# Performance work log

Measured on AMD Instinct MI355X. Metric: run time of the kernel, lower is better.

## Reference

```python
import jax, jax.numpy as jnp
import numpy as np

B, S, T = 256, 120, 24   # batch, src frames, predicted frames
D, H = 216, 1024          # input_dim (24 joints x 3x3 rotmat), hidden_dim


def setup_inputs() -> dict:
    key = jax.random.key(0)
    ks = jax.random.split(key, 8)
    s = 0.05  # ~ init_weights uniform(-0.08, 0.08) scale
    return {
        "src": jax.random.normal(ks[0], (B, S, D), jnp.float32),
        "tgt": jax.random.normal(ks[1], (B, T, D), jnp.float32),
        "W_ih": jax.random.normal(ks[2], (4 * H, D), jnp.float32) * s,
        "W_hh": jax.random.normal(ks[3], (4 * H, H), jnp.float32) * s,
        "b_ih": jnp.zeros((4 * H,), jnp.float32),
        "b_hh": jnp.zeros((4 * H,), jnp.float32),
        "W_out": jax.random.normal(ks[4], (D, H), jnp.float32) * s,
        "b_out": jnp.zeros((D,), jnp.float32),
        "max_len": T,
    }


def reference(src, tgt, W_ih, W_hh, b_ih, b_hh, W_out, b_out, max_len):
    # Eval-mode forward: dropout = identity.
    # Encoder: teacher-forced (teacher_forcing_ratio=1.0 -> always feed src[t]).
    def cell(x, h, c):
        # PyTorch LSTM gate order: i, f, g, o
        gates = x @ W_ih.T + b_ih + h @ W_hh.T + b_hh  # [B, 4H]
        i, f, g, o = jnp.split(gates, 4, axis=-1)
        c = jax.nn.sigmoid(f) * c + jax.nn.sigmoid(i) * jnp.tanh(g)
        h = jax.nn.sigmoid(o) * jnp.tanh(c)
        return h, c

    b = src.shape[0]
    h0 = jnp.zeros((b, H), src.dtype)
    c0 = jnp.zeros((b, H), src.dtype)

    # Encoder over src, time-major [S, B, D]
    def enc_step(carry, x):
        h, c = carry
        h, c = cell(x, h, c)
        return (h, c), None

    (h, c), _ = jax.lax.scan(enc_step, (h0, c0), jnp.swapaxes(src, 0, 1))

    # Decoder: first input is last src frame, then feed back projected output
    def dec_step(carry, _):
        h, c, x = carry
        h, c = cell(x, h, c)
        out = h @ W_out.T + b_out  # [B, D]
        return (h, c, out), out

    _, outs = jax.lax.scan(dec_step, (h, c, src[:, -1, :]), None, length=max_len)
    return jnp.swapaxes(outs, 0, 1)  # [B, max_len, D]
```

## Files before the change

kernel.cpp:

```cpp
#include <hip/hip_runtime.h>
#include <hip/hip_bf16.h>

typedef unsigned short u16;
typedef unsigned int   u32;
typedef unsigned long long u64;
typedef __attribute__((ext_vector_type(4)))  float  f32x4;
typedef __attribute__((ext_vector_type(8)))  short  short8;
typedef __attribute__((ext_vector_type(16))) float  f32x16;

#define MB     256
#define SRCT   120
#define DECT   24
#define NSTEP  144
#define DIN    216
#define HDIM   1024
#define KXP    224
#define KA     1248
#define NGATE  4096
#define OUTD   216
#define NWG    256

#define OFF_SRCBF 0u
#define OFF_H     13762560u
#define OFF_XDEC  14811136u
#define OFF_WCAT  14925824u
#define OFF_WO    25149440u
#define OFF_BAR   25591808u

__device__ __forceinline__ u16 f2bf(float f) {
    union { float f; unsigned v; } c; c.f = f;
    return (u16)((c.v + 0x7FFFu + ((c.v >> 16) & 1u)) >> 16);
}
__device__ __forceinline__ float sigm(float x)  { return 1.0f / (1.0f + __expf(-x)); }
__device__ __forceinline__ float tanh_(float x) { return 1.0f - 2.0f / (1.0f + __expf(2.0f * x)); }

__device__ __forceinline__ void astore(u64* p, u64 v) {
    __hip_atomic_store(p, v, __ATOMIC_RELAXED, __HIP_MEMORY_SCOPE_AGENT);
}

__device__ __forceinline__ short8 ld_sc(const u16* p) {
    short8 r;
    asm volatile("global_load_dwordx4 %0, %1, off sc0 sc1" : "=v"(r) : "v"(p));
    return r;
}
template <int N>
__device__ __forceinline__ void vwait() {
    asm volatile("s_waitcnt vmcnt(%0)" :: "n"(N));
    __builtin_amdgcn_sched_barrier(0);
}

__device__ __forceinline__ void g_arrive(u32* slots, int k) {
    __syncthreads();
    if (threadIdx.x == 0)
        __hip_atomic_fetch_add(slots + (k & 63), 1u, __ATOMIC_RELAXED, __HIP_MEMORY_SCOPE_AGENT);
}
__device__ __forceinline__ void g_wait(u32* slots, int k) {
    if (threadIdx.x == 0) {
        const u32 tgt = 32u * (u32)((k >> 6) + 1);
        while (__hip_atomic_load(slots + (k & 63), __ATOMIC_RELAXED, __HIP_MEMORY_SCOPE_AGENT) < tgt)
            __builtin_amdgcn_s_sleep(1);
    }
    __syncthreads();
}

__global__ void prep_kernel(const float* __restrict__ src,
                            const float* __restrict__ W_ih,
                            const float* __restrict__ W_hh,
                            const float* __restrict__ W_out,
                            u16* __restrict__ srcbf, u16* __restrict__ H,
                            u16* __restrict__ Xd,    u16* __restrict__ Wcat,
                            u16* __restrict__ Wo,    u32* __restrict__ bar) {
    const int nS  = SRCT * 8 * 28 * 256;
    const int nW  = NGATE * KA;
    const int nWo = OUTD * HDIM;
    const int nH  = MB * HDIM;
    const int nXd = 8 * 28 * 256;
    const int nB  = 8 * 64;
    const int total = nS + nW + nWo + nH + nXd + nB;
    for (int i = blockIdx.x * blockDim.x + threadIdx.x; i < total; i += gridDim.x * blockDim.x) {
        if (i < nS) {
            int r = i & 255, i2 = i >> 8;
            int m = r >> 3, e = r & 7;
            int oct = i2 % 28, q = i2 / 28;
            int gi = q & 7, t = q >> 3;
            int col = oct * 8 + e, b = gi * 32 + m;
            srcbf[i] = (col < DIN) ? f2bf(src[((size_t)b * SRCT + t) * DIN + col]) : (u16)0;
        } else if (i < nS + nW) {
            int j = i - nS;
            int r = j / KA, col = j % KA;
            u16 v = 0;
            if (col < DIN)       v = f2bf(W_ih[(size_t)r * DIN + col]);
            else if (col >= KXP) v = f2bf(W_hh[(size_t)r * HDIM + (col - KXP)]);
            Wcat[j] = v;
        } else if (i < nS + nW + nWo) {
            int j = i - nS - nW;
            Wo[j] = f2bf(W_out[j]);
        } else if (i < nS + nW + nWo + nH) {
            H[i - nS - nW - nWo] = 0;
        } else if (i < nS + nW + nWo + nH + nXd) {
            Xd[i - nS - nW - nWo - nH] = 0;
        } else {
            bar[i - nS - nW - nWo - nH - nXd] = 0;
        }
    }
}

template <int J>
__device__ __forceinline__ void gate_issue(short8 (&av)[20], const u16* xb, const u16* hb,
                                           int ktb, int lo) {
    int kt = ktb + J;
    if (kt > 77) kt = 77;
    const int o2 = 2 * kt;
    const u16* base = (o2 < 28) ? (xb + o2 * 256) : (hb + (o2 - 28) * 256);
    av[J] = ld_sc(base + lo);
}
template <int J>
__device__ __forceinline__ void gate_pro(short8 (&av)[20], const u16* xb, const u16* hb,
                                         int ktb, int lo) {
    gate_issue<J>(av, xb, hb, ktb, lo);
    if constexpr (J + 1 < 8) gate_pro<J + 1>(av, xb, hb, ktb, lo);
}
template <int J>
__device__ __forceinline__ void gate_body(short8 (&av)[20], short8 (&Bf)[4][20], f32x16 (&acc)[4],
                                          const u16* xb, const u16* hb, int ktb, int lo) {
    if constexpr (J + 8 < 20) gate_issue<J + 8>(av, xb, hb, ktb, lo);
    vwait<(J + 8 < 20) ? 8 : (19 - J)>();
    acc[0] = __builtin_amdgcn_mfma_f32_32x32x16_bf16(av[J], Bf[0][J], acc[0], 0, 0, 0);
    acc[1] = __builtin_amdgcn_mfma_f32_32x32x16_bf16(av[J], Bf[1][J], acc[1], 0, 0, 0);
    acc[2] = __builtin_amdgcn_mfma_f32_32x32x16_bf16(av[J], Bf[2][J], acc[2], 0, 0, 0);
    acc[3] = __builtin_amdgcn_mfma_f32_32x32x16_bf16(av[J], Bf[3][J], acc[3], 0, 0, 0);
    if constexpr (J + 1 < 20) gate_body<J + 1>(av, Bf, acc, xb, hb, ktb, lo);
}

template <int J>
__device__ __forceinline__ void out_issue(short8 (&av)[16], const u16* hb, int kt0, int lo) {
    const int o2 = 2 * (kt0 + J);
    av[J] = ld_sc(hb + o2 * 256 + lo);
}
template <int J>
__device__ __forceinline__ void out_pro(short8 (&av)[16], const u16* hb, int kt0, int lo) {
    out_issue<J>(av, hb, kt0, lo);
    if constexpr (J + 1 < 8) out_pro<J + 1>(av, hb, kt0, lo);
}
template <int J>
__device__ __forceinline__ void out_body(short8 (&av)[16], f32x16& oacc, const u16* hb,
                                         const u16* wob, int kt0, int lo) {
    if constexpr (J + 8 < 16) out_issue<J + 8>(av, hb, kt0, lo);
    vwait<(J + 8 < 16) ? 8 : (15 - J)>();
    short8 bf = *(const short8*)(wob + (size_t)(kt0 + J) * 16);
    oacc = __builtin_amdgcn_mfma_f32_32x32x16_bf16(av[J], bf, oacc, 0, 0, 0);
    if constexpr (J + 1 < 16) out_body<J + 1>(av, oacc, hb, wob, kt0, lo);
}

__global__ void __launch_bounds__(256, 1)
lstm_persist(const u16* __restrict__ srcbf, u16* __restrict__ H,
             u16* __restrict__ Xd, const u16* __restrict__ Wcat,
             const u16* __restrict__ Wo,
             const float* __restrict__ b_ih, const float* __restrict__ b_hh,
             const float* __restrict__ b_out,
             float* __restrict__ dout, u32* __restrict__ bar)
{
    __shared__ __align__(16) float G2[16 * 32 * 36];
    __shared__ __align__(16) u16  Hx[4 * 32 * 8];
    __shared__ __align__(16) char lds_pad[8192];

    const int bid  = blockIdx.x;
    const int g    = bid & 7;
    const int s    = bid >> 3;
    const int b0   = g * 32;
    const int tid  = threadIdx.x;
    const int p    = tid >> 6;
    const int lane = tid & 63;
    const int l31  = lane & 31;
    const int kg   = lane >> 5;
    const int lo   = kg * 256 + l31 * 8;

    if (tid == 255) *(volatile char*)lds_pad = 0;

    u32* gslots = bar + g * 64;
    u16* Xdg = Xd + (size_t)g * 7168;

    const int ktb = p * 20 - (p == 3 ? 1 : 0);
    const int ktc = (p < 2) ? 20 : 19;

    short8 Bfrag[4][20];
#pragma unroll
    for (int gg = 0; gg < 4; ++gg) {
        const u16* pw = Wcat + (size_t)(gg * 1024 + s * 32 + l31) * KA + kg * 8;
#pragma unroll
        for (int j = 0; j < 20; ++j) {
            if (j < ktc) {
                int kt = ktb + j;
                Bfrag[gg][j] = *(const short8*)(pw + (size_t)kt * 16);
            } else {
                Bfrag[gg][j] = short8{};
            }
        }
    }

    const int cs = tid & 31;
    const int bq = tid >> 5;
    float creg[4] = {0.f, 0.f, 0.f, 0.f};
    const int hcg = s * 32 + cs;
    const float bI  = b_ih[hcg]        + b_hh[hcg];
    const float bF  = b_ih[1024 + hcg] + b_hh[1024 + hcg];
    const float bG_ = b_ih[2048 + hcg] + b_hh[2048 + hcg];
    const float bO  = b_ih[3072 + hcg] + b_hh[3072 + hcg];
    const float bOutv = (s < 7 && hcg < OUTD) ? b_out[hcg] : 0.f;

    for (int t = 0; t < NSTEP; ++t) {
        const u16* hb    = H + (size_t)(t & 1) * (MB * HDIM) + (size_t)g * 32768;
        u16*       HTn   = H + (size_t)((t + 1) & 1) * (MB * HDIM);
        const u16* hnext = HTn + (size_t)g * 32768;
        const u16* xb;
        if (t < SRCT)       xb = srcbf + (size_t)(t * 8 + g) * 7168;
        else if (t == SRCT) xb = srcbf + (size_t)((SRCT - 1) * 8 + g) * 7168;
        else                xb = Xdg;

        f32x16 acc[4] = {f32x16{}, f32x16{}, f32x16{}, f32x16{}};
        {
            short8 av[20];
            gate_pro<0>(av, xb, hb, ktb, lo);
            gate_body<0>(av, Bfrag, acc, xb, hb, ktb, lo);
        }
#pragma unroll
        for (int gg = 0; gg < 4; ++gg) {
#pragma unroll
            for (int rq = 0; rq < 4; ++rq) {
                f32x4 v;
                v[0] = acc[gg][rq * 4 + 0]; v[1] = acc[gg][rq * 4 + 1];
                v[2] = acc[gg][rq * 4 + 2]; v[3] = acc[gg][rq * 4 + 3];
                *(f32x4*)&G2[(size_t)((gg * 4 + p) * 32 + l31) * 36 + rq * 8 + kg * 4] = v;
            }
        }
        __syncthreads();

        {
            f32x4 sg[4];
#pragma unroll
            for (int gg = 0; gg < 4; ++gg) {
                f32x4 a = *(const f32x4*)&G2[(size_t)((gg * 4 + 0) * 32 + cs) * 36 + bq * 4];
#pragma unroll
                for (int pp = 1; pp < 4; ++pp)
                    a += *(const f32x4*)&G2[(size_t)((gg * 4 + pp) * 32 + cs) * 36 + bq * 4];
                sg[gg] = a;
            }
#pragma unroll
            for (int i = 0; i < 4; ++i) {
                float gi = sg[0][i] + bI, gf = sg[1][i] + bF;
                float gG = sg[2][i] + bG_, go = sg[3][i] + bO;
                float c = sigm(gf) * creg[i] + sigm(gi) * tanh_(gG);
                creg[i] = c;
                Hx[(cs >> 3) * 256 + (bq * 4 + i) * 8 + (cs & 7)] = f2bf(sigm(go) * tanh_(c));
            }
        }
        __syncthreads();
        astore((u64*)HTn + (size_t)g * 8192 + s * 256 + tid, ((const u64*)Hx)[tid]);

        if (t < SRCT) {
            g_arrive(gslots, t);
            g_wait(gslots, t);
        } else {
            const int d  = t - SRCT;
            const int k1 = SRCT + 2 * d;
            g_arrive(gslots, k1);
            g_wait(gslots, k1);
            if (s < 7) {
                f32x16 oacc = {};
                const int orow = (s * 32 + l31 < OUTD) ? (s * 32 + l31) : (OUTD - 1);
                const u16* wob = Wo + (size_t)orow * HDIM + kg * 8;
                short8 av2[16];
                out_pro<0>(av2, hnext, p * 16, lo);
                out_body<0>(av2, oacc, hnext, wob, p * 16, lo);
#pragma unroll
                for (int rq = 0; rq < 4; ++rq) {
                    f32x4 v;
                    v[0] = oacc[rq * 4 + 0]; v[1] = oacc[rq * 4 + 1];
                    v[2] = oacc[rq * 4 + 2]; v[3] = oacc[rq * 4 + 3];
                    *(f32x4*)&G2[(size_t)(p * 32 + l31) * 36 + rq * 8 + kg * 4] = v;
                }
            }
            __syncthreads();
            if (s < 7) {
                const int  ocol = s * 32 + cs;
                const bool real = ocol < OUTD;
                f32x4 S = *(const f32x4*)&G2[(size_t)(0 * 32 + cs) * 36 + bq * 4];
#pragma unroll
                for (int pp = 1; pp < 4; ++pp)
                    S += *(const f32x4*)&G2[(size_t)(pp * 32 + cs) * 36 + bq * 4];
#pragma unroll
                for (int i = 0; i < 4; ++i) {
                    float v = real ? (S[i] + bOutv) : 0.f;
                    Hx[(cs >> 3) * 256 + (bq * 4 + i) * 8 + (cs & 7)] = real ? f2bf(v) : (u16)0;
                    if (real)
                        dout[(size_t)(b0 + bq * 4 + i) * (DECT * OUTD) + (size_t)d * OUTD + ocol] = v;
                }
            }
            __syncthreads();
            if (s < 7)
                astore((u64*)Xdg + s * 256 + tid, ((const u64*)Hx)[tid]);
            if (t < NSTEP - 1) {
                g_arrive(gslots, k1 + 1);
                g_wait(gslots, k1 + 1);
            }
        }
    }
}

extern "C" void kernel_launch(void* const* d_in, const int* in_sizes, int n_in,
                              void* d_out, int out_size, void* d_ws, size_t ws_size,
                              hipStream_t stream) {
    const float* src   = (const float*)d_in[0];
    const float* W_ih  = (const float*)d_in[2];
    const float* W_hh  = (const float*)d_in[3];
    const float* b_ih  = (const float*)d_in[4];
    const float* b_hh  = (const float*)d_in[5];
    const float* W_out = (const float*)d_in[6];
    const float* b_out = (const float*)d_in[7];
    float* out = (float*)d_out;

    char* ws = (char*)d_ws;
    u16* srcbf = (u16*)(ws + OFF_SRCBF);
    u16* H     = (u16*)(ws + OFF_H);
    u16* Xd    = (u16*)(ws + OFF_XDEC);
    u16* Wcat  = (u16*)(ws + OFF_WCAT);
    u16* Wo    = (u16*)(ws + OFF_WO);
    u32* bar   = (u32*)(ws + OFF_BAR);

    hipLaunchKernelGGL(prep_kernel, dim3(2048), dim3(256), 0, stream,
                       src, W_ih, W_hh, W_out, srcbf, H, Xd, Wcat, Wo, bar);

    hipLaunchKernelGGL(lstm_persist, dim3(NWG), dim3(256), 0, stream,
                       srcbf, H, Xd, Wcat, Wo, b_ih, b_hh, b_out, out, bar);
}
```

Measured before the change: 868.9 us.

## Map batch groups to XCCs and use L2-coherent loads/stores for hidden state

Each workgroup now reads its hardware XCC ID and takes an atomic ticket, so a 32-row batch group and its barrier all sit on one XCC and share its L2. With that placement, hidden-state loads drop the system-coherent sc1 bit and stores become plain stores, with an explicit vmcnt(0) wait before the barrier arrive. This is meant to cut cross-die coherence traffic on every recurrent step. It relies on exactly 32 workgroups landing on each XCC and on using the Xd buffer as ticket counters, which risks wrong indices or a hang if scheduling differs.

```diff
diff --git a/kernel.cpp b/kernel.cpp
--- a/kernel.cpp
+++ b/kernel.cpp
@@ -34,13 +34,11 @@
 __device__ __forceinline__ float sigm(float x)  { return 1.0f / (1.0f + __expf(-x)); }
 __device__ __forceinline__ float tanh_(float x) { return 1.0f - 2.0f / (1.0f + __expf(2.0f * x)); }
 
-__device__ __forceinline__ void astore(u64* p, u64 v) {
-    __hip_atomic_store(p, v, __ATOMIC_RELAXED, __HIP_MEMORY_SCOPE_AGENT);
-}
-
-__device__ __forceinline__ short8 ld_sc(const u16* p) {
+__device__ __forceinline__ void pstore(u64* p, u64 v) { *p = v; }
+
+__device__ __forceinline__ short8 ld_l2(const u16* p) {
     short8 r;
-    asm volatile("global_load_dwordx4 %0, %1, off sc0 sc1" : "=v"(r) : "v"(p));
+    asm volatile("global_load_dwordx4 %0, %1, off sc0" : "=v"(r) : "v"(p));
     return r;
 }
 template <int N>
@@ -51,8 +49,10 @@
 
 __device__ __forceinline__ void g_arrive(u32* slots, int k) {
     __syncthreads();
-    if (threadIdx.x == 0)
+    if (threadIdx.x == 0) {
+        asm volatile("s_waitcnt vmcnt(0)" ::: "memory");
         __hip_atomic_fetch_add(slots + (k & 63), 1u, __ATOMIC_RELAXED, __HIP_MEMORY_SCOPE_AGENT);
+    }
 }
 __device__ __forceinline__ void g_wait(u32* slots, int k) {
     if (threadIdx.x == 0) {
@@ -112,7 +112,7 @@
     if (kt > 77) kt = 77;
     const int o2 = 2 * kt;
     const u16* base = (o2 < 28) ? (xb + o2 * 256) : (hb + (o2 - 28) * 256);
-    av[J] = ld_sc(base + lo);
+    av[J] = ld_l2(base + lo);
 }
 template <int J>
 __device__ __forceinline__ void gate_pro(short8 (&av)[20], const u16* xb, const u16* hb,
@@ -135,7 +135,7 @@
 template <int J>
 __device__ __forceinline__ void out_issue(short8 (&av)[16], const u16* hb, int kt0, int lo) {
     const int o2 = 2 * (kt0 + J);
-    av[J] = ld_sc(hb + o2 * 256 + lo);
+    av[J] = ld_l2(hb + o2 * 256 + lo);
 }
 template <int J>
 __device__ __forceinline__ void out_pro(short8 (&av)[16], const u16* hb, int kt0, int lo) {
@@ -163,11 +163,8 @@
     __shared__ __align__(16) float G2[16 * 32 * 36];
     __shared__ __align__(16) u16  Hx[4 * 32 * 8];
     __shared__ __align__(16) char lds_pad[8192];
-
-    const int bid  = blockIdx.x;
-    const int g    = bid & 7;
-    const int s    = bid >> 3;
-    const int b0   = g * 32;
+    __shared__ int gs_share[2];
+
     const int tid  = threadIdx.x;
     const int p    = tid >> 6;
     const int lane = tid & 63;
@@ -176,6 +173,19 @@
     const int lo   = kg * 256 + l31 * 8;
 
     if (tid == 255) *(volatile char*)lds_pad = 0;
+
+    if (tid == 0) {
+        u32 xcc;
+        asm volatile("s_getreg_b32 %0, hwreg(HW_REG_XCC_ID)" : "=s"(xcc));
+        u32 myidx = __hip_atomic_fetch_add((u32*)Xd + xcc, 1u,
+                                           __ATOMIC_RELAXED, __HIP_MEMORY_SCOPE_AGENT);
+        gs_share[0] = (int)xcc;
+        gs_share[1] = (int)myidx;
+    }
+    __syncthreads();
+    const int g  = gs_share[0];
+    const int s  = gs_share[1];
+    const int b0 = g * 32;
 
     u32* gslots = bar + g * 64;
     u16* Xdg = Xd + (size_t)g * 7168;
@@ -255,7 +265,7 @@
             }
         }
         __syncthreads();
-        astore((u64*)HTn + (size_t)g * 8192 + s * 256 + tid, ((const u64*)Hx)[tid]);
+        pstore((u64*)HTn + (size_t)g * 8192 + s * 256 + tid, ((const u64*)Hx)[tid]);
 
         if (t < SRCT) {
             g_arrive(gslots, t);
@@ -298,7 +308,7 @@
             }
             __syncthreads();
             if (s < 7)
-                astore((u64*)Xdg + s * 256 + tid, ((const u64*)Hx)[tid]);
+                pstore((u64*)Xdg + s * 256 + tid, ((const u64*)Hx)[tid]);
             if (t < NSTEP - 1) {
                 g_arrive(gslots, k1 + 1);
                 g_wait(gslots, k1 + 1);
```

New measurement: 860.3 us. About the same (-1.0%).
